# Kernel tuning notes

Measured on AMD Instinct MI355X. Metric: run time of the kernel, lower is better.

The kernel has to match this reference:

```python
import jax, jax.numpy as jnp
import numpy as np
import math

HID = 1152
NH = 16
HD = HID // NH            # 72
P = 2
DEPTH = 4
MLP_M = int(2.0 / 3.0 * int(HID * 4.0))  # 3072 (SwiGLU inner)
FREQ = 256
NCLS = 1000
ROPE_THETA = 10000.0


def rms_norm(x, w, eps=1e-6):
    return x * jax.lax.rsqrt(jnp.mean(jnp.square(x), axis=-1, keepdims=True) + eps) * w


def rotate_half(x):
    # interleaved pairs (a, b) -> (-b, a)
    x2 = x.reshape(x.shape[:-1] + (x.shape[-1] // 2, 2))
    a, b = x2[..., 0], x2[..., 1]
    return jnp.stack((-b, a), axis=-1).reshape(x.shape)


def make_rope(S, head_dim, theta=ROPE_THETA):
    # VisionRotaryEmbedder: per-axis rope dim = head_dim//2, 2 spatial axes concat
    d = head_dim // 2
    f = 1.0 / theta ** (jnp.arange(0, d, 2)[: d // 2].astype(jnp.float32) / d)
    fr = jnp.arange(S, dtype=jnp.float32)[:, None] * f[None, :]   # [S, d//2]
    fr = jnp.repeat(fr, 2, axis=-1)                               # [S, d]
    grid = jnp.concatenate(
        [jnp.broadcast_to(fr[:, None, :], (S, S, d)),
         jnp.broadcast_to(fr[None, :, :], (S, S, d))], axis=-1)   # [S, S, head_dim]
    grid = grid.reshape(S * S, head_dim)
    return jnp.cos(grid), jnp.sin(grid)


def timestep_embedding(t, dim=FREQ, max_period=10000.0):
    half = dim // 2
    freqs = jnp.exp(-math.log(max_period) * jnp.arange(half, dtype=jnp.float32) / half)
    args = t[:, None].astype(jnp.float32) * freqs[None, :]
    return jnp.concatenate([jnp.cos(args), jnp.sin(args)], axis=-1)


def setup_inputs() -> dict:
    key = jax.random.key(0)
    ks = jax.random.split(key, 24)
    s = 0.02
    B, C, H, W = 2, 4, 64, 64
    d = {
        'x': jax.random.normal(ks[0], (B, C, H, W), jnp.float32),
        't': jax.random.uniform(ks[1], (B,), jnp.float32),
        'y': jax.random.randint(ks[2], (B,), 0, NCLS),
        'patch_w': jax.random.normal(ks[3], (P * P * C, HID), jnp.float32) * s,
        'patch_b': jnp.zeros((HID,), jnp.float32),
        't_w1': jax.random.normal(ks[4], (FREQ, HID), jnp.float32) * s,
        't_b1': jnp.zeros((HID,), jnp.float32),
        't_w2': jax.random.normal(ks[5], (HID, HID), jnp.float32) * s,
        't_b2': jnp.zeros((HID,), jnp.float32),
        'y_table': jax.random.normal(ks[6], (NCLS + 1, HID), jnp.float32) * s,
        'norm1_w': jnp.ones((DEPTH, HID), jnp.float32),
        'qkv_w': jax.random.normal(ks[7], (DEPTH, HID, 3 * HID), jnp.float32) * s,
        'qkv_b': jnp.zeros((DEPTH, 3 * HID), jnp.float32),
        'out_w': jax.random.normal(ks[8], (DEPTH, HID, HID), jnp.float32) * s,
        'out_b': jnp.zeros((DEPTH, HID), jnp.float32),
        'norm2_w': jnp.ones((DEPTH, HID), jnp.float32),
        'mlp_w12': jax.random.normal(ks[9], (DEPTH, HID, 2 * MLP_M), jnp.float32) * s,
        'mlp_b12': jnp.zeros((DEPTH, 2 * MLP_M), jnp.float32),
        'mlp_w3': jax.random.normal(ks[10], (DEPTH, MLP_M, HID), jnp.float32) * s,
        'mlp_b3': jnp.zeros((DEPTH, HID), jnp.float32),
        'adaln_w': jax.random.normal(ks[11], (DEPTH, HID, 4 * HID), jnp.float32) * s,
        'adaln_b': jnp.zeros((DEPTH, 4 * HID), jnp.float32),
        'fnorm_w': jnp.ones((HID,), jnp.float32),
        'fadaln_w': jax.random.normal(ks[12], (HID, 2 * HID), jnp.float32) * s,
        'fadaln_b': jnp.zeros((2 * HID,), jnp.float32),
        'flin_w': jax.random.normal(ks[13], (HID, P * P * C), jnp.float32) * s,
        'flin_b': jnp.zeros((P * P * C,), jnp.float32),
    }
    return d


def reference(x, t, y, patch_w, patch_b, t_w1, t_b1, t_w2, t_b2, y_table,
              norm1_w, qkv_w, qkv_b, out_w, out_b, norm2_w,
              mlp_w12, mlp_b12, mlp_w3, mlp_b3, adaln_w, adaln_b,
              fnorm_w, fadaln_w, fadaln_b, flin_w, flin_b):
    B, C, H, W = x.shape
    S = H // P
    L = S * S
    # patchify -> [B, L, P*P*C] -> linear embed
    tok = x.reshape(B, C, S, P, S, P).transpose(0, 2, 4, 3, 5, 1).reshape(B, L, P * P * C)
    h = tok @ patch_w + patch_b
    # conditioning: timestep MLP + class embedding
    temb = timestep_embedding(t)
    temb = jax.nn.silu(temb @ t_w1 + t_b1) @ t_w2 + t_b2
    c = temb + y_table[y]
    c_silu = jax.nn.silu(c)
    cos, sin = make_rope(S, HD)  # [L, HD]
    scale = 1.0 / math.sqrt(HD)

    def block(hx, p):
        n1w, qw, qb, ow, ob, n2w, w12, b12, w3, b3, aw, ab = p
        mod = c_silu @ aw + ab  # [B, 4*HID]
        s_msa, g_msa, s_mlp, g_mlp = jnp.split(mod, 4, axis=-1)
        hmod = rms_norm(hx, n1w) * (1.0 + s_msa[:, None, :])
        qkv = (hmod @ qw + qb).reshape(B, L, 3, NH, HD)
        qkv = jnp.swapaxes(qkv, 1, 3)  # [B, NH, 3, L, HD]
        q, k, v = qkv[:, :, 0], qkv[:, :, 1], qkv[:, :, 2]
        q = q * cos + rotate_half(q) * sin
        k = k * cos + rotate_half(k) * sin
        w = jax.nn.softmax(jnp.einsum('bhqd,bhkd->bhqk', q, k) * scale, axis=-1)
        o = jnp.einsum('bhqk,bhkd->bhqd', w, v)
        o = jnp.swapaxes(o, 1, 2).reshape(B, L, HID) @ ow + ob
        hx = hx + g_msa[:, None, :] * o
        hmod2 = rms_norm(hx, n2w) * (1.0 + s_mlp[:, None, :])
        x12 = hmod2 @ w12 + b12
        x1, x2 = jnp.split(x12, 2, axis=-1)
        m = (jax.nn.silu(x1) * x2) @ w3 + b3
        hx = hx + g_mlp[:, None, :] * m
        return hx, None

    h, _ = jax.lax.scan(block, h, (norm1_w, qkv_w, qkv_b, out_w, out_b, norm2_w,
                                   mlp_w12, mlp_b12, mlp_w3, mlp_b3, adaln_w, adaln_b))

    # final layer: shift+scale modulation then zero-init linear (random here)
    fmod = c_silu @ fadaln_w + fadaln_b
    shift, fscale = jnp.split(fmod, 2, axis=-1)
    hf = rms_norm(h, fnorm_w) * (1.0 + fscale[:, None, :]) + shift[:, None, :]
    out = hf @ flin_w + flin_b  # [B, L, P*P*C]
    out = out.reshape(B, S, S, P, P, C).transpose(0, 5, 1, 3, 2, 4).reshape(B, C, H, W)
    return out
```

## Files before the change

### kernel.cpp

```cpp
#include <hip/hip_runtime.h>
#include <hip/hip_bf16.h>

#define HIDN 1152
#define NHEAD 16
#define HDIM 72
#define LTOK 1024
#define MTOK 2048
#define MLPM 3072

typedef short bf16x8 __attribute__((ext_vector_type(8)));
typedef float f32x4 __attribute__((ext_vector_type(4)));

__device__ __forceinline__ void gload16(const void* g, void* l) {
    __builtin_amdgcn_global_load_lds(
        (const __attribute__((address_space(1))) void*)g,
        (__attribute__((address_space(3))) void*)l,
        16, 0, 0);
}

__global__ __launch_bounds__(256) void k_patch(const float* __restrict__ x,
        const float* __restrict__ pw, const float* __restrict__ pb,
        float* __restrict__ h) {
    int m = blockIdx.x;
    int b = m >> 10, l = m & 1023;
    int si = l >> 5, sj = l & 31;
    __shared__ float toks[16];
    int tid = threadIdx.x;
    if (tid < 16) {
        int pi = tid >> 3, pj = (tid >> 2) & 1, c = tid & 3;
        toks[tid] = x[((size_t)(b*4 + c)*64 + si*2 + pi)*64 + sj*2 + pj];
    }
    __syncthreads();
    for (int o = tid; o < HIDN; o += 256) {
        float acc = pb[o];
        #pragma unroll
        for (int kk = 0; kk < 16; ++kk) acc += toks[kk] * pw[kk*HIDN + o];
        h[(size_t)m*HIDN + o] = acc;
    }
}

__global__ __launch_bounds__(256) void k_temb1_v2(const float* __restrict__ t,
        const float* __restrict__ w1, const float* __restrict__ b1,
        float* __restrict__ temb1) {
    int jt = blockIdx.x, b = blockIdx.y;
    int tid = threadIdx.x;
    __shared__ float emb[256];
    __shared__ float red[128];
    float tv = t[b];
    if (tid < 128) { float f = __expf(-logf(10000.f) * (float)tid / 128.f);        emb[tid] = cosf(tv * f); }
    else           { float f = __expf(-logf(10000.f) * (float)(tid - 128) / 128.f); emb[tid] = sinf(tv * f); }
    __syncthreads();
    int o = jt*128 + (tid & 127), s = tid >> 7;
    float acc = 0.f;
    for (int k = s*128; k < s*128 + 128; ++k) acc += emb[k] * w1[(size_t)k*HIDN + o];
    if (s) red[tid & 127] = acc;
    __syncthreads();
    if (!s) {
        float v = acc + red[tid] + b1[o];
        temb1[b*HIDN + o] = v / (1.f + __expf(-v));
    }
}

__global__ __launch_bounds__(256) void k_csilu_s1(const float* __restrict__ temb1,
        const float* __restrict__ w2, float* __restrict__ csilup) {
    int jt = blockIdx.x, kz = blockIdx.y;
    int tid = threadIdx.x;
    __shared__ float t1s[2][288];
    __shared__ float red[2][128];
    for (int i = tid; i < 576; i += 256)
        t1s[i/288][i%288] = temb1[(i/288)*HIDN + kz*288 + (i%288)];
    __syncthreads();
    int o = jt*128 + (tid & 127), s = tid >> 7;
    float a0 = 0.f, a1 = 0.f;
    for (int i = s*144; i < s*144 + 144; ++i) {
        float wv = w2[(size_t)(kz*288 + i)*HIDN + o];
        a0 += t1s[0][i]*wv; a1 += t1s[1][i]*wv;
    }
    if (s) { red[0][tid & 127] = a0; red[1][tid & 127] = a1; }
    __syncthreads();
    if (!s) {
        csilup[(kz*2 + 0)*HIDN + o] = a0 + red[0][tid];
        csilup[(kz*2 + 1)*HIDN + o] = a1 + red[1][tid];
    }
}

__global__ __launch_bounds__(128) void k_csilu_s2(const float* __restrict__ csilup,
        const float* __restrict__ b2, const float* __restrict__ ytab,
        const int* __restrict__ y, float* __restrict__ csilu) {
    int o = blockIdx.x*128 + threadIdx.x;
    int b = blockIdx.y;
    float acc = b2[o] + ytab[(size_t)y[b]*HIDN + o];
    #pragma unroll
    for (int kz = 0; kz < 4; ++kz) acc += csilup[(kz*2 + b)*HIDN + o];
    csilu[b*HIDN + o] = acc / (1.f + __expf(-acc));
}

__global__ __launch_bounds__(256) void k_cond_s1(const float* __restrict__ csilu,
        const float* __restrict__ adaln_w, const float* __restrict__ fadaln_w,
        float* __restrict__ condp) {
    int ct = blockIdx.x, kz = blockIdx.y;
    int tid = threadIdx.x;
    int c0 = ct*128;
    const float* Wb; int rstride;
    if (c0 < 18432) { int d = c0/4608; Wb = adaln_w + (size_t)d*HIDN*4608 + (c0 % 4608); rstride = 4608; }
    else            { Wb = fadaln_w + (c0 - 18432); rstride = 2304; }
    __shared__ float cs[2][288];
    __shared__ float red[2][128];
    for (int i = tid; i < 576; i += 256)
        cs[i/288][i%288] = csilu[(i/288)*HIDN + kz*288 + (i%288)];
    __syncthreads();
    int o = tid & 127, s = tid >> 7;
    float a0 = 0.f, a1 = 0.f;
    for (int i = s*144; i < s*144 + 144; ++i) {
        float wv = Wb[(size_t)(kz*288 + i)*rstride + o];
        a0 += cs[0][i]*wv; a1 += cs[1][i]*wv;
    }
    if (s) { red[0][o] = a0; red[1][o] = a1; }
    __syncthreads();
    if (!s) {
        condp[((size_t)kz*2 + 0)*20736 + c0 + o] = a0 + red[0][o];
        condp[((size_t)kz*2 + 1)*20736 + c0 + o] = a1 + red[1][o];
    }
}

__global__ __launch_bounds__(256) void k_cond_s2(const float* __restrict__ condp,
        const float* __restrict__ adaln_b, const float* __restrict__ fadaln_b,
        float* __restrict__ modb, float* __restrict__ fmod) {
    int c = blockIdx.x*256 + threadIdx.x;
    int b = blockIdx.y;
    float acc = 0.f;
    #pragma unroll
    for (int kz = 0; kz < 4; ++kz) acc += condp[((size_t)kz*2 + b)*20736 + c];
    if (c < 18432) {
        int d = c/4608, j = c%4608;
        modb[((size_t)d*2 + b)*4608 + j] = acc + adaln_b[(size_t)d*4608 + j];
    } else {
        int j = c - 18432;
        fmod[(size_t)b*2304 + j] = acc + fadaln_b[j];
    }
}

__global__ __launch_bounds__(256) void k_rope(float* __restrict__ cosb, float* __restrict__ sinb) {
    int idx = blockIdx.x*256 + threadIdx.x;
    if (idx >= LTOK*HDIM) return;
    int l = idx / HDIM, dd = idx % HDIM;
    int i = l >> 5, j = l & 31;
    int pos = (dd < 36) ? i : j;
    int mm = ((dd < 36) ? dd : dd - 36) >> 1;
    float f = __expf(-logf(10000.f) * (float)mm / 18.f);
    float fr = (float)pos * f;
    cosb[idx] = cosf(fr);
    sinb[idx] = sinf(fr);
}

__global__ __launch_bounds__(256) void k_rms(const float* __restrict__ hx,
        const float* __restrict__ nw, const float* __restrict__ smod,
        __hip_bfloat16* __restrict__ outp) {
    int m = blockIdx.x; int b = m >> 10;
    int tid = threadIdx.x;
    const float* row = hx + (size_t)m*HIDN;
    float part = 0.f;
    for (int j = tid; j < HIDN; j += 256) { float v = row[j]; part += v*v; }
    for (int off = 32; off; off >>= 1) part += __shfl_xor(part, off);
    __shared__ float wsum[4];
    if ((tid & 63) == 0) wsum[tid >> 6] = part;
    __syncthreads();
    float rs = rsqrtf((wsum[0]+wsum[1]+wsum[2]+wsum[3]) * (1.f/HIDN) + 1e-6f);
    const float* sb = smod + (size_t)b*4608;
    __hip_bfloat16* orow = outp + (size_t)m*HIDN;
    for (int j = tid; j < HIDN; j += 256)
        orow[j] = __float2bfloat16(row[j] * rs * nw[j] * (1.f + sb[j]));
}

__global__ __launch_bounds__(256) void k_castT(const float* __restrict__ W,
        __hip_bfloat16* __restrict__ Wt, int K, int N) {
    __shared__ float tile[32][33];
    int n0 = blockIdx.x*32, k0 = blockIdx.y*32;
    int tx = threadIdx.x, ty = threadIdx.y;
    for (int i = ty; i < 32; i += 8)
        tile[i][tx] = W[(size_t)(k0+i)*N + n0 + tx];
    __syncthreads();
    for (int i = ty; i < 32; i += 8)
        Wt[(size_t)(n0+i)*K + k0 + tx] = __float2bfloat16(tile[tx][i]);
}

template<int EPI, typename OutT>
__global__ __launch_bounds__(256) void k_gemm_bf16(
        const __hip_bfloat16* __restrict__ A,
        const __hip_bfloat16* __restrict__ Wt,
        const float* __restrict__ bias,
        OutT* __restrict__ C, int M, int N, int K,
        const float* __restrict__ gate) {
    __shared__ __hip_bfloat16 Asm[128*64];
    __shared__ __hip_bfloat16 Bsm[128*64];
    int tid = threadIdx.x;
    int lane = tid & 63, w = tid >> 6;
    int wr = w >> 1, wc = w & 1;
    int m0 = blockIdx.y * 128, n0 = blockIdx.x * 128;
    f32x4 acc[4][4] = {};
    int lr = lane >> 3, ls = lane & 7;
    int swz = ls ^ (lr & 7);
    int x7 = lane & 7;
    const __hip_bfloat16* Ag = A  + (size_t)(m0 + lr)*K + swz*8;
    const __hip_bfloat16* Bg = Wt + (size_t)(n0 + lr)*K + swz*8;
    for (int k0 = 0; k0 < K; k0 += 64) {
        #pragma unroll
        for (int i = 0; i < 4; ++i) {
            int seg = w*4 + i;
            gload16(Ag + (size_t)(seg*8)*K + k0, (char*)Asm + seg*1024);
            gload16(Bg + (size_t)(seg*8)*K + k0, (char*)Bsm + seg*1024);
        }
        __syncthreads();
        #pragma unroll
        for (int kk = 0; kk < 2; ++kk) {
            bf16x8 af[4], bfr[4];
            #pragma unroll
            for (int m = 0; m < 4; ++m) {
                int row = wr*64 + m*16 + (lane&15);
                af[m] = *(const bf16x8*)(Asm + row*64 + (((kk*4 + (lane>>4)) ^ x7) * 8));
            }
            #pragma unroll
            for (int n = 0; n < 4; ++n) {
                int col = wc*64 + n*16 + (lane&15);
                bfr[n] = *(const bf16x8*)(Bsm + col*64 + (((kk*4 + (lane>>4)) ^ x7) * 8));
            }
            #pragma unroll
            for (int m = 0; m < 4; ++m)
                #pragma unroll
                for (int n = 0; n < 4; ++n)
                    acc[m][n] = __builtin_amdgcn_mfma_f32_16x16x32_bf16(af[m], bfr[n], acc[m][n], 0, 0, 0);
        }
        __syncthreads();
    }
    int r0 = (lane >> 4) * 4;
    int ccol = lane & 15;
    #pragma unroll
    for (int m = 0; m < 4; ++m) {
        #pragma unroll
        for (int rr = 0; rr < 4; ++rr) {
            int row = m0 + wr*64 + m*16 + r0 + rr;
            int bi = row >> 10;
            #pragma unroll
            for (int n = 0; n < 4; ++n) {
                int col = n0 + wc*64 + n*16 + ccol;
                float val = acc[m][n][rr] + bias[col];
                if (EPI == 0) {
                    C[(size_t)row*N + col] = (OutT)__float2bfloat16(val);
                } else {
                    ((float*)C)[(size_t)row*N + col] += gate[(size_t)bi*4608 + col] * val;
                }
            }
        }
    }
}

__global__ __launch_bounds__(256) void k_gemm64(
        const __hip_bfloat16* __restrict__ A,
        const __hip_bfloat16* __restrict__ Wt,
        const float* __restrict__ bias,
        float* __restrict__ C, int M, int N, int K,
        const float* __restrict__ gate) {
    __shared__ __hip_bfloat16 Asm[64*64];
    __shared__ __hip_bfloat16 Bsm[128*64];
    int tid = threadIdx.x;
    int lane = tid & 63, w = tid >> 6;
    int wr = w >> 1, wc = w & 1;
    int m0 = blockIdx.y * 64, n0 = blockIdx.x * 128;
    f32x4 acc[2][4] = {};
    int lr = lane >> 3, ls = lane & 7;
    int swz = ls ^ (lr & 7);
    int x7 = lane & 7;
    const __hip_bfloat16* Ag = A  + (size_t)(m0 + lr)*K + swz*8;
    const __hip_bfloat16* Bg = Wt + (size_t)(n0 + lr)*K + swz*8;
    for (int k0 = 0; k0 < K; k0 += 64) {
        #pragma unroll
        for (int i = 0; i < 2; ++i) {
            int seg = w*2 + i;
            gload16(Ag + (size_t)(seg*8)*K + k0, (char*)Asm + seg*1024);
        }
        #pragma unroll
        for (int i = 0; i < 4; ++i) {
            int seg = w*4 + i;
            gload16(Bg + (size_t)(seg*8)*K + k0, (char*)Bsm + seg*1024);
        }
        __syncthreads();
        #pragma unroll
        for (int kk = 0; kk < 2; ++kk) {
            bf16x8 af[2], bfr[4];
            #pragma unroll
            for (int m = 0; m < 2; ++m) {
                int row = wr*32 + m*16 + (lane&15);
                af[m] = *(const bf16x8*)(Asm + row*64 + (((kk*4 + (lane>>4)) ^ x7) * 8));
            }
            #pragma unroll
            for (int n = 0; n < 4; ++n) {
                int col = wc*64 + n*16 + (lane&15);
                bfr[n] = *(const bf16x8*)(Bsm + col*64 + (((kk*4 + (lane>>4)) ^ x7) * 8));
            }
            #pragma unroll
            for (int m = 0; m < 2; ++m)
                #pragma unroll
                for (int n = 0; n < 4; ++n)
                    acc[m][n] = __builtin_amdgcn_mfma_f32_16x16x32_bf16(af[m], bfr[n], acc[m][n], 0, 0, 0);
        }
        __syncthreads();
    }
    int r0 = (lane >> 4) * 4;
    int ccol = lane & 15;
    #pragma unroll
    for (int m = 0; m < 2; ++m) {
        #pragma unroll
        for (int rr = 0; rr < 4; ++rr) {
            int row = m0 + wr*32 + m*16 + r0 + rr;
            int bi = row >> 10;
            #pragma unroll
            for (int n = 0; n < 4; ++n) {
                int col = n0 + wc*64 + n*16 + ccol;
                float val = acc[m][n][rr] + bias[col];
                C[(size_t)row*N + col] += gate[(size_t)bi*4608 + col] * val;
            }
        }
    }
}

__global__ __launch_bounds__(256) void k_ropesplit(const __hip_bfloat16* __restrict__ qkv,
        const float* __restrict__ cosb, const float* __restrict__ sinb,
        __hip_bfloat16* __restrict__ q, __hip_bfloat16* __restrict__ k,
        __hip_bfloat16* __restrict__ v) {
    int idx = blockIdx.x*256 + threadIdx.x;
    if (idx >= 2*NHEAD*LTOK*36) return;
    int dp = idx % 36;
    int l  = (idx / 36) % LTOK;
    int h  = (idx / (36*LTOK)) % NHEAD;
    int b  = idx / (36*LTOK*NHEAD);
    int d0 = dp*2;
    size_t src = (size_t)(b*LTOK + l)*3456 + h*HDIM + d0;
    float qe = __bfloat162float(qkv[src]),        qo = __bfloat162float(qkv[src+1]);
    float ke = __bfloat162float(qkv[src+HIDN]),   ko = __bfloat162float(qkv[src+HIDN+1]);
    float ce = cosb[l*HDIM+d0], co = cosb[l*HDIM+d0+1];
    float se = sinb[l*HDIM+d0], so = sinb[l*HDIM+d0+1];
    size_t dst = (size_t)((b*NHEAD + h)*LTOK + l)*HDIM + d0;
    q[dst]   = __float2bfloat16(qe*ce - qo*se);
    q[dst+1] = __float2bfloat16(qo*co + qe*so);
    k[dst]   = __float2bfloat16(ke*ce - ko*se);
    k[dst+1] = __float2bfloat16(ko*co + ke*so);
    size_t vdst = ((size_t)(b*NHEAD + h)*HDIM + d0)*LTOK + l;
    v[vdst]        = qkv[src+2*HIDN];
    v[vdst+LTOK]   = qkv[src+2*HIDN+1];
}

__global__ __launch_bounds__(256) void k_attn_mfma(
        const __hip_bfloat16* __restrict__ q,
        const __hip_bfloat16* __restrict__ k,
        const __hip_bfloat16* __restrict__ vt,
        __hip_bfloat16* __restrict__ o) {
    int blk = blockIdx.x;
    int qt = blk & 15, h = (blk >> 4) & 15, b = blk >> 8;
    const float scale = 0.117851130f;
    __shared__ __hip_bfloat16 Ksm[64*104];
    __shared__ __hip_bfloat16 Vsm[80*72];
    __shared__ __hip_bfloat16 Psm[4][16*72];
    int tid = threadIdx.x, lane = tid & 63, w = tid >> 6;
    int l15 = lane & 15, g = lane >> 4;
    const __hip_bfloat16* qg = q  + ((size_t)(b*NHEAD + h)*LTOK + qt*64)*HDIM;
    const __hip_bfloat16* kg = k  + (size_t)(b*NHEAD + h)*LTOK*HDIM;
    const __hip_bfloat16* vg = vt + (size_t)(b*NHEAD + h)*HDIM*LTOK;

    {
        bf16x8 z = {};
        *(bf16x8*)(Ksm + (tid>>2)*104 + 72 + (tid&3)*8) = z;
        if (tid < 72) *(bf16x8*)(Vsm + (72 + tid/9)*72 + (tid%9)*8) = z;
    }
    for (int i = tid; i < 576; i += 256) {
        int r = i/9, s = i%9;
        *(bf16x8*)(Ksm + r*104 + s*8) = *(const bf16x8*)(qg + r*HDIM + s*8);
    }
    __syncthreads();
    bf16x8 qf[3];
    #pragma unroll
    for (int c = 0; c < 3; ++c)
        qf[c] = *(const bf16x8*)(Ksm + (w*16 + l15)*104 + c*32 + g*8);
    __syncthreads();

    f32x4 oacc[5] = {};
    float mold[4] = {-1e30f, -1e30f, -1e30f, -1e30f};
    float lsum[4] = {};

    for (int kt = 0; kt < 16; ++kt) {
        for (int i = tid; i < 576; i += 256) {
            int r = i/9, s = i%9;
            *(bf16x8*)(Ksm + r*104 + s*8) = *(const bf16x8*)(kg + (size_t)(kt*64 + r)*HDIM + s*8);
        }
        for (int i = tid; i < 576; i += 256) {
            int r = i>>3, s = i&7;
            *(bf16x8*)(Vsm + r*72 + s*8) = *(const bf16x8*)(vg + (size_t)r*LTOK + kt*64 + s*8);
        }
        __syncthreads();
        f32x4 st[4] = {};
        #pragma unroll
        for (int t = 0; t < 4; ++t) {
            #pragma unroll
            for (int c = 0; c < 3; ++c) {
                bf16x8 kf = *(const bf16x8*)(Ksm + (t*16 + l15)*104 + c*32 + g*8);
                st[t] = __builtin_amdgcn_mfma_f32_16x16x32_bf16(qf[c], kf, st[t], 0, 0, 0);
            }
        }
        #pragma unroll
        for (int r = 0; r < 4; ++r) {
            float mt = fmaxf(fmaxf(st[0][r], st[1][r]), fmaxf(st[2][r], st[3][r]));
            mt = fmaxf(mt, __shfl_xor(mt, 1));
            mt = fmaxf(mt, __shfl_xor(mt, 2));
            mt = fmaxf(mt, __shfl_xor(mt, 4));
            mt = fmaxf(mt, __shfl_xor(mt, 8));
            float mn = fmaxf(mold[r], mt);
            float corr = __expf((mold[r] - mn) * scale);
            mold[r] = mn;
            lsum[r] *= corr;
            #pragma unroll
            for (int dt = 0; dt < 5; ++dt) oacc[dt][r] *= corr;
            float rs = 0.f;
            #pragma unroll
            for (int t = 0; t < 4; ++t) {
                float p = __expf((st[t][r] - mn) * scale);
                rs += p;
                Psm[w][(g*4 + r)*72 + t*16 + l15] = __float2bfloat16(p);
            }
            rs += __shfl_xor(rs, 1);
            rs += __shfl_xor(rs, 2);
            rs += __shfl_xor(rs, 4);
            rs += __shfl_xor(rs, 8);
            lsum[r] += rs;
        }
        bf16x8 pa[2];
        #pragma unroll
        for (int c = 0; c < 2; ++c)
            pa[c] = *(const bf16x8*)(&Psm[w][l15*72 + c*32 + g*8]);
        #pragma unroll
        for (int dt = 0; dt < 5; ++dt) {
            #pragma unroll
            for (int c = 0; c < 2; ++c) {
                bf16x8 vf = *(const bf16x8*)(Vsm + (dt*16 + l15)*72 + c*32 + g*8);
                oacc[dt] = __builtin_amdgcn_mfma_f32_16x16x32_bf16(pa[c], vf, oacc[dt], 0, 0, 0);
            }
        }
        __syncthreads();
    }
    #pragma unroll
    for (int r = 0; r < 4; ++r) {
        float inv = 1.f / lsum[r];
        int row = qt*64 + w*16 + g*4 + r;
        __hip_bfloat16* op = o + ((size_t)b*LTOK + row)*HIDN + h*HDIM;
        #pragma unroll
        for (int dt = 0; dt < 5; ++dt) {
            int d = dt*16 + l15;
            if (d < HDIM) op[d] = __float2bfloat16(oacc[dt][r] * inv);
        }
    }
}

__global__ __launch_bounds__(256) void k_glu(const __hip_bfloat16* __restrict__ x12,
        __hip_bfloat16* __restrict__ mh) {
    int idx = blockIdx.x*256 + threadIdx.x;
    int m = idx / 384, jj = (idx % 384)*8;
    bf16x8 v1 = *(const bf16x8*)(x12 + (size_t)m*6144 + jj);
    bf16x8 v2 = *(const bf16x8*)(x12 + (size_t)m*6144 + MLPM + jj);
    bf16x8 ov;
    #pragma unroll
    for (int i = 0; i < 8; ++i) {
        short s1 = v1[i], s2 = v2[i];
        float x1 = __bfloat162float(*(__hip_bfloat16*)&s1);
        float x2 = __bfloat162float(*(__hip_bfloat16*)&s2);
        __hip_bfloat16 r = __float2bfloat16(x1 / (1.f + __expf(-x1)) * x2);
        ov[i] = *(short*)&r;
    }
    *(bf16x8*)(mh + (size_t)m*MLPM + jj) = ov;
}

__global__ __launch_bounds__(256) void k_final(const float* __restrict__ hx,
        const float* __restrict__ fnw, const float* __restrict__ fmod,
        const float* __restrict__ flw, const float* __restrict__ flb,
        float* __restrict__ out) {
    int m = blockIdx.x; int b = m >> 10, l = m & 1023;
    int tid = threadIdx.x;
    const float* row = hx + (size_t)m*HIDN;
    float part = 0.f;
    for (int j = tid; j < HIDN; j += 256) { float v2 = row[j]; part += v2*v2; }
    for (int off = 32; off; off >>= 1) part += __shfl_xor(part, off);
    __shared__ float wsum[4];
    __shared__ float hfs[HIDN];
    __shared__ float red[4][16];
    if ((tid & 63) == 0) wsum[tid >> 6] = part;
    __syncthreads();
    float rs = rsqrtf((wsum[0]+wsum[1]+wsum[2]+wsum[3]) * (1.f/HIDN) + 1e-6f);
    const float* fm = fmod + (size_t)b*2304;
    for (int j = tid; j < HIDN; j += 256)
        hfs[j] = row[j] * rs * fnw[j] * (1.f + fm[HIDN + j]) + fm[j];
    __syncthreads();
    float pacc[16] = {};
    for (int j = tid; j < HIDN; j += 256) {
        float hv = hfs[j];
        #pragma unroll
        for (int kk = 0; kk < 16; ++kk) pacc[kk] += hv * flw[j*16 + kk];
    }
    #pragma unroll
    for (int kk = 0; kk < 16; ++kk)
        for (int off = 32; off; off >>= 1) pacc[kk] += __shfl_xor(pacc[kk], off);
    if ((tid & 63) == 0) {
        int w = tid >> 6;
        #pragma unroll
        for (int kk = 0; kk < 16; ++kk) red[w][kk] = pacc[kk];
    }
    __syncthreads();
    if (tid < 16) {
        float val = red[0][tid] + red[1][tid] + red[2][tid] + red[3][tid] + flb[tid];
        int pi = tid >> 3, pj = (tid >> 2) & 1, c = tid & 3;
        int si = l >> 5, sj = l & 31;
        out[((size_t)(b*4 + c)*64 + si*2 + pi)*64 + sj*2 + pj] = val;
    }
}

extern "C" void kernel_launch(void* const* d_in, const int* in_sizes, int n_in,
                              void* d_out, int out_size, void* d_ws, size_t ws_size,
                              hipStream_t stream) {
    const float* x        = (const float*)d_in[0];
    const float* t        = (const float*)d_in[1];
    const int*   y        = (const int*)  d_in[2];
    const float* patch_w  = (const float*)d_in[3];
    const float* patch_b  = (const float*)d_in[4];
    const float* t_w1     = (const float*)d_in[5];
    const float* t_b1     = (const float*)d_in[6];
    const float* t_w2     = (const float*)d_in[7];
    const float* t_b2     = (const float*)d_in[8];
    const float* y_table  = (const float*)d_in[9];
    const float* norm1_w  = (const float*)d_in[10];
    const float* qkv_w    = (const float*)d_in[11];
    const float* qkv_b    = (const float*)d_in[12];
    const float* out_w    = (const float*)d_in[13];
    const float* out_b    = (const float*)d_in[14];
    const float* norm2_w  = (const float*)d_in[15];
    const float* mlp_w12  = (const float*)d_in[16];
    const float* mlp_b12  = (const float*)d_in[17];
    const float* mlp_w3   = (const float*)d_in[18];
    const float* mlp_b3   = (const float*)d_in[19];
    const float* adaln_w  = (const float*)d_in[20];
    const float* adaln_b  = (const float*)d_in[21];
    const float* fnorm_w  = (const float*)d_in[22];
    const float* fadaln_w = (const float*)d_in[23];
    const float* fadaln_b = (const float*)d_in[24];
    const float* flin_w   = (const float*)d_in[25];
    const float* flin_b   = (const float*)d_in[26];

    char* base = (char*)d_ws;
    float*          hx    = (float*)(base);
    __hip_bfloat16* qkvbf = (__hip_bfloat16*)(base +  9437184);
    __hip_bfloat16* qbf   = (__hip_bfloat16*)(base + 34603008);
    __hip_bfloat16* kbf   = (__hip_bfloat16*)(base + 39321600);
    __hip_bfloat16* vbf   = (__hip_bfloat16*)(base + 44040192);
    __hip_bfloat16* hbf   = (__hip_bfloat16*)(base + 48758784);
    __hip_bfloat16* mhbf  = qbf;
    __hip_bfloat16* wtb   = (__hip_bfloat16*)(base + 53477376);
    float* temb1 = (float*)(base + 85327872);
    float* csilu = (float*)(base + 85337088);
    float* modb  = (float*)(base + 85346304);
    float* fmod  = (float*)(base + 85493760);
    float* cosb  = (float*)(base + 85512192);
    float* sinb  = (float*)(base + 85807104);
    float* condp = (float*)(base + 86102016);
    float* csilup= (float*)(base + 86765568);

    __hip_bfloat16* wt_qkv = wtb;
    __hip_bfloat16* wt_out = wt_qkv + 3456*1152;
    __hip_bfloat16* wt_m12 = wt_out + 1152*1152;
    __hip_bfloat16* wt_m3  = wt_m12 + 6144*1152;

    k_patch<<<2048, 256, 0, stream>>>(x, patch_w, patch_b, hx);
    k_temb1_v2<<<dim3(9,2), 256, 0, stream>>>(t, t_w1, t_b1, temb1);
    k_csilu_s1<<<dim3(9,4), 256, 0, stream>>>(temb1, t_w2, csilup);
    k_csilu_s2<<<dim3(9,2), 128, 0, stream>>>(csilup, t_b2, y_table, y, csilu);
    k_cond_s1<<<dim3(162,4), 256, 0, stream>>>(csilu, adaln_w, fadaln_w, condp);
    k_cond_s2<<<dim3(81,2), 256, 0, stream>>>(condp, adaln_b, fadaln_b, modb, fmod);
    k_rope<<<288, 256, 0, stream>>>(cosb, sinb);

    for (int d = 0; d < 4; ++d) {
        const float* modd = modb + (size_t)d*2*4608;
        k_castT<<<dim3(108,36), dim3(32,8), 0, stream>>>(qkv_w  + (size_t)d*HIDN*3456, wt_qkv, HIDN, 3456);
        k_castT<<<dim3( 36,36), dim3(32,8), 0, stream>>>(out_w  + (size_t)d*HIDN*HIDN, wt_out, HIDN, HIDN);
        k_castT<<<dim3(192,36), dim3(32,8), 0, stream>>>(mlp_w12+ (size_t)d*HIDN*6144, wt_m12, HIDN, 6144);
        k_castT<<<dim3( 36,96), dim3(32,8), 0, stream>>>(mlp_w3 + (size_t)d*MLPM*HIDN, wt_m3,  MLPM, HIDN);

        k_rms<<<2048, 256, 0, stream>>>(hx, norm1_w + d*HIDN, modd + 0*HIDN, hbf);
        k_gemm_bf16<0, __hip_bfloat16><<<dim3(27,16), 256, 0, stream>>>(hbf, wt_qkv,
                qkv_b + d*3456, qkvbf, MTOK, 3456, HIDN, nullptr);
        k_ropesplit<<<4608, 256, 0, stream>>>(qkvbf, cosb, sinb, qbf, kbf, vbf);
        k_attn_mfma<<<512, 256, 0, stream>>>(qbf, kbf, vbf, hbf);
        k_gemm64<<<dim3(9,32), 256, 0, stream>>>(hbf, wt_out,
                out_b + d*HIDN, hx, MTOK, HIDN, HIDN, modd + 1*HIDN);
        k_rms<<<2048, 256, 0, stream>>>(hx, norm2_w + d*HIDN, modd + 2*HIDN, hbf);
        k_gemm_bf16<0, __hip_bfloat16><<<dim3(48,16), 256, 0, stream>>>(hbf, wt_m12,
                mlp_b12 + d*6144, qkvbf, MTOK, 6144, HIDN, nullptr);
        k_glu<<<3072, 256, 0, stream>>>(qkvbf, mhbf);
        k_gemm64<<<dim3(9,32), 256, 0, stream>>>(mhbf, wt_m3,
                mlp_b3 + d*HIDN, hx, MTOK, HIDN, MLPM, modd + 3*HIDN);
    }
    k_final<<<2048, 256, 0, stream>>>(hx, fnorm_w, fmod, flin_w, flin_b, (float*)d_out);
}
```

Measured before the change: 1.171 ms.

## Double-buffer attention K/V tiles with async global-to-LDS loads and swizzled V layout

Rewrites the attention K/V staging to use global_load_lds (direct-to-LDS) into double-buffered shared memory. The next tile is prefetched while the current one is computed, and the per-tile barrier before compute is removed. Q fragments are now loaded straight from global memory, the K padding columns are replaced by zeroed register fragments, and V uses an XOR swizzle to avoid LDS bank conflicts. s_setprio hints are also added around the MFMA blocks. This aims to hide global load latency, but it relies on the single end-of-loop barrier to order the async loads, with no explicit vmcnt wait.

```diff
diff --git a/kernel.cpp b/kernel.cpp
--- a/kernel.cpp
+++ b/kernel.cpp
@@ -357,54 +357,65 @@
     int blk = blockIdx.x;
     int qt = blk & 15, h = (blk >> 4) & 15, b = blk >> 8;
     const float scale = 0.117851130f;
-    __shared__ __hip_bfloat16 Ksm[64*104];
-    __shared__ __hip_bfloat16 Vsm[80*72];
+    __shared__ __hip_bfloat16 Ksm[2][64*72];
+    __shared__ __hip_bfloat16 Vsm[2][72*64];
     __shared__ __hip_bfloat16 Psm[4][16*72];
     int tid = threadIdx.x, lane = tid & 63, w = tid >> 6;
     int l15 = lane & 15, g = lane >> 4;
     const __hip_bfloat16* qg = q  + ((size_t)(b*NHEAD + h)*LTOK + qt*64)*HDIM;
     const __hip_bfloat16* kg = k  + (size_t)(b*NHEAD + h)*LTOK*HDIM;
     const __hip_bfloat16* vg = vt + (size_t)(b*NHEAD + h)*HDIM*LTOK;
-
+    const bf16x8 z = {};
+
+    bf16x8 qf[3];
     {
-        bf16x8 z = {};
-        *(bf16x8*)(Ksm + (tid>>2)*104 + 72 + (tid&3)*8) = z;
-        if (tid < 72) *(bf16x8*)(Vsm + (72 + tid/9)*72 + (tid%9)*8) = z;
-    }
-    for (int i = tid; i < 576; i += 256) {
-        int r = i/9, s = i%9;
-        *(bf16x8*)(Ksm + r*104 + s*8) = *(const bf16x8*)(qg + r*HDIM + s*8);
-    }
-    __syncthreads();
-    bf16x8 qf[3];
-    #pragma unroll
-    for (int c = 0; c < 3; ++c)
-        qf[c] = *(const bf16x8*)(Ksm + (w*16 + l15)*104 + c*32 + g*8);
-    __syncthreads();
+        const __hip_bfloat16* qrow = qg + (w*16 + l15)*HDIM;
+        qf[0] = *(const bf16x8*)(qrow + g*8);
+        qf[1] = *(const bf16x8*)(qrow + 32 + g*8);
+        qf[2] = (g == 0) ? *(const bf16x8*)(qrow + 64) : z;
+    }
+    int vsw  = ((lane & 7) ^ (lane >> 3)) * 8;
+    int vrow = lane >> 3;
 
     f32x4 oacc[5] = {};
     float mold[4] = {-1e30f, -1e30f, -1e30f, -1e30f};
     float lsum[4] = {};
 
-    for (int kt = 0; kt < 16; ++kt) {
-        for (int i = tid; i < 576; i += 256) {
-            int r = i/9, s = i%9;
-            *(bf16x8*)(Ksm + r*104 + s*8) = *(const bf16x8*)(kg + (size_t)(kt*64 + r)*HDIM + s*8);
-        }
-        for (int i = tid; i < 576; i += 256) {
-            int r = i>>3, s = i&7;
-            *(bf16x8*)(Vsm + r*72 + s*8) = *(const bf16x8*)(vg + (size_t)r*LTOK + kt*64 + s*8);
-        }
-        __syncthreads();
+    {
+        const __hip_bfloat16* ktg = kg;
+        const __hip_bfloat16* vtg = vg;
+        for (int s = w; s < 9; s += 4) {
+            gload16(ktg + s*512 + lane*8, (char*)&Ksm[0][0] + s*1024);
+            gload16(vtg + (size_t)(s*8 + vrow)*LTOK + vsw, (char*)&Vsm[0][0] + s*1024);
+        }
+    }
+    __syncthreads();
+
+    for (int kt2 = 0; kt2 < 16; ++kt2) {
+        int cur = kt2 & 1;
+        if (kt2 < 15) {
+            const __hip_bfloat16* ktg = kg + (size_t)(kt2+1)*64*HDIM;
+            const __hip_bfloat16* vtg = vg + (kt2+1)*64;
+            for (int s = w; s < 9; s += 4) {
+                gload16(ktg + s*512 + lane*8, (char*)&Ksm[cur^1][0] + s*1024);
+                gload16(vtg + (size_t)(s*8 + vrow)*LTOK + vsw, (char*)&Vsm[cur^1][0] + s*1024);
+            }
+        }
+        const __hip_bfloat16* Kc = Ksm[cur];
+        const __hip_bfloat16* Vc = Vsm[cur];
         f32x4 st[4] = {};
+        __builtin_amdgcn_s_setprio(1);
         #pragma unroll
         for (int t = 0; t < 4; ++t) {
-            #pragma unroll
-            for (int c = 0; c < 3; ++c) {
-                bf16x8 kf = *(const bf16x8*)(Ksm + (t*16 + l15)*104 + c*32 + g*8);
-                st[t] = __builtin_amdgcn_mfma_f32_16x16x32_bf16(qf[c], kf, st[t], 0, 0, 0);
-            }
-        }
+            const __hip_bfloat16* krow = Kc + (t*16 + l15)*72;
+            bf16x8 kf0 = *(const bf16x8*)(krow + g*8);
+            bf16x8 kf1 = *(const bf16x8*)(krow + 32 + g*8);
+            bf16x8 kf2 = (g == 0) ? *(const bf16x8*)(krow + 64) : z;
+            st[t] = __builtin_amdgcn_mfma_f32_16x16x32_bf16(qf[0], kf0, st[t], 0, 0, 0);
+            st[t] = __builtin_amdgcn_mfma_f32_16x16x32_bf16(qf[1], kf1, st[t], 0, 0, 0);
+            st[t] = __builtin_amdgcn_mfma_f32_16x16x32_bf16(qf[2], kf2, st[t], 0, 0, 0);
+        }
+        __builtin_amdgcn_s_setprio(0);
         #pragma unroll
         for (int r = 0; r < 4; ++r) {
             float mt = fmaxf(fmaxf(st[0][r], st[1][r]), fmaxf(st[2][r], st[3][r]));
@@ -431,18 +442,20 @@
             rs += __shfl_xor(rs, 8);
             lsum[r] += rs;
         }
-        bf16x8 pa[2];
-        #pragma unroll
-        for (int c = 0; c < 2; ++c)
-            pa[c] = *(const bf16x8*)(&Psm[w][l15*72 + c*32 + g*8]);
+        bf16x8 pa0 = *(const bf16x8*)(&Psm[w][l15*72 + g*8]);
+        bf16x8 pa1 = *(const bf16x8*)(&Psm[w][l15*72 + 32 + g*8]);
+        int cswz = (l15 & 7)*8;
+        __builtin_amdgcn_s_setprio(1);
         #pragma unroll
         for (int dt = 0; dt < 5; ++dt) {
-            #pragma unroll
-            for (int c = 0; c < 2; ++c) {
-                bf16x8 vf = *(const bf16x8*)(Vsm + (dt*16 + l15)*72 + c*32 + g*8);
-                oacc[dt] = __builtin_amdgcn_mfma_f32_16x16x32_bf16(pa[c], vf, oacc[dt], 0, 0, 0);
-            }
-        }
+            int row = dt*16 + l15;
+            bool valid = (dt < 4) | (l15 < 8);
+            bf16x8 vf0 = valid ? *(const bf16x8*)(Vc + row*64 + ((g*8) ^ cswz)) : z;
+            bf16x8 vf1 = valid ? *(const bf16x8*)(Vc + row*64 + ((32 + g*8) ^ cswz)) : z;
+            oacc[dt] = __builtin_amdgcn_mfma_f32_16x16x32_bf16(pa0, vf0, oacc[dt], 0, 0, 0);
+            oacc[dt] = __builtin_amdgcn_mfma_f32_16x16x32_bf16(pa1, vf1, oacc[dt], 0, 0, 0);
+        }
+        __builtin_amdgcn_s_setprio(0);
         __syncthreads();
     }
     #pragma unroll
```

New measurement: 1.097 ms. -6.3%, faster.
